# Kernel optimization log

Measured on AMD Instinct MI355X. Metric: run time of the kernel, lower is better.

## Reference

```python
import jax, jax.numpy as jnp
import numpy as np

DIM = 4096
N_HEADS = 32
N_KV_HEADS = 8
HEAD_DIM = DIM // N_HEADS  # 128
B, S = 2, 2048
LN_EPS = 1e-5


def _precompute_freqs_cis(seqlen, head_dim, theta=10000.0):
    inv = 1.0 / (theta ** (np.arange(0, head_dim, 2, dtype=np.float32) / head_dim))  # [HD/2]
    ang = np.outer(np.arange(seqlen, dtype=np.float32), inv)  # [S, HD/2]
    return jnp.asarray(np.stack([np.cos(ang), np.sin(ang)], axis=-1))  # [S, HD/2, 2]


def setup_inputs() -> dict:
    key = jax.random.key(0)
    ks = jax.random.split(key, 9)
    std = 0.02
    return {
        "x": jax.random.normal(ks[0], (B, S, DIM), dtype=jnp.float32),
        "freqs_cis": _precompute_freqs_cis(S, HEAD_DIM),
        "wq": jax.random.normal(ks[1], (N_HEADS * HEAD_DIM, DIM), dtype=jnp.float32) * std,
        "wk": jax.random.normal(ks[2], (N_KV_HEADS * HEAD_DIM, DIM), dtype=jnp.float32) * std,
        "wv": jax.random.normal(ks[3], (N_KV_HEADS * HEAD_DIM, DIM), dtype=jnp.float32) * std,
        "wo": jax.random.normal(ks[4], (DIM, N_HEADS * HEAD_DIM), dtype=jnp.float32) * std,
        "q_norm_w": jnp.ones((N_HEADS * HEAD_DIM,), dtype=jnp.float32),
        "q_norm_b": jnp.zeros((N_HEADS * HEAD_DIM,), dtype=jnp.float32),
        "k_norm_w": jnp.ones((N_KV_HEADS * HEAD_DIM,), dtype=jnp.float32),
        "k_norm_b": jnp.zeros((N_KV_HEADS * HEAD_DIM,), dtype=jnp.float32),
    }


def _layernorm(v, w, b):
    mu = jnp.mean(v, axis=-1, keepdims=True)
    var = jnp.var(v, axis=-1, keepdims=True)
    return (v - mu) * jax.lax.rsqrt(var + LN_EPS) * w + b


def _rope(t, fc):
    # t: [B, S, nh, HD]; fc: [S, HD/2, 2] = (cos, sin)
    b_, s_, nh, hd = t.shape
    tr = t.reshape(b_, s_, nh, hd // 2, 2)
    a, bb = tr[..., 0], tr[..., 1]
    cos = fc[None, :, None, :, 0]
    sin = fc[None, :, None, :, 1]
    out = jnp.stack([a * cos - bb * sin, a * sin + bb * cos], axis=-1)
    return out.reshape(t.shape)


def reference(x, freqs_cis, wq, wk, wv, wo, q_norm_w, q_norm_b, k_norm_w, k_norm_b):
    bsz, seqlen, _ = x.shape
    H, KV, HD = N_HEADS, N_KV_HEADS, HEAD_DIM
    R = H // KV  # GQA repeat factor

    xq = jnp.einsum('bsd,ed->bse', x, wq)
    xk = jnp.einsum('bsd,ed->bse', x, wk)
    xv = jnp.einsum('bsd,ed->bse', x, wv)

    xq = _layernorm(xq, q_norm_w, q_norm_b)
    xk = _layernorm(xk, k_norm_w, k_norm_b)

    xq = xq.reshape(bsz, seqlen, H, HD)
    xk = xk.reshape(bsz, seqlen, KV, HD)
    xv = xv.reshape(bsz, seqlen, KV, HD)

    xq = _rope(xq, freqs_cis)
    xk = _rope(xk, freqs_cis)

    # GQA: group q heads as (kv, rep) and broadcast k/v instead of materializing repeats
    xqg = xq.reshape(bsz, seqlen, KV, R, HD)
    scale = 1.0 / jnp.sqrt(jnp.float32(HD))
    scores = jnp.einsum('bqkrh,bskh->bkrqs', xqg, xk) * scale  # [B,KV,R,S,S]
    attn = jax.nn.softmax(scores, axis=-1)
    out = jnp.einsum('bkrqs,bskh->bqkrh', attn, xv).reshape(bsz, seqlen, H * HD)
    return jnp.einsum('bse,de->bsd', out, wo)
```

## Files before the change

kernel.cpp:

```cpp
#include <hip/hip_runtime.h>
#include <cstdint>

typedef _Float16 half4v __attribute__((ext_vector_type(4)));
typedef _Float16 half8v __attribute__((ext_vector_type(8)));
typedef __fp16   fp16x2 __attribute__((ext_vector_type(2)));
typedef float    f32x4v __attribute__((ext_vector_type(4)));

#define DIM    4096
#define SEQ    2048
#define NBATCH 2
#define NHEAD  32
#define NKVH   8
#define HDIM   128
#define MROWS  (NBATCH*SEQ)
#define QKV_N  6144
#define KOFF   4096
#define VOFF   5120

__device__ __forceinline__ void gl_lds16(const void* g, void* l) {
  __builtin_amdgcn_global_load_lds(
      (const __attribute__((address_space(1))) void*)g,
      (__attribute__((address_space(3))) void*)l, 16, 0, 0);
}

__global__ __launch_bounds__(256) void cvt_kernel(const float* __restrict__ in,
                                                  _Float16* __restrict__ out, int n8) {
  int stride = gridDim.x * blockDim.x;
  for (int i = blockIdx.x * blockDim.x + threadIdx.x; i < n8; i += stride) {
    const float4* p = (const float4*)(in + (size_t)i * 8);
    float4 a = p[0], b = p[1];
    half8v h;
    h[0] = (_Float16)a.x; h[1] = (_Float16)a.y; h[2] = (_Float16)a.z; h[3] = (_Float16)a.w;
    h[4] = (_Float16)b.x; h[5] = (_Float16)b.y; h[6] = (_Float16)b.z; h[7] = (_Float16)b.w;
    *(half8v*)(out + (size_t)i * 8) = h;
  }
}


#define SBAR() do { asm volatile("" ::: "memory"); \
                    __builtin_amdgcn_s_barrier();  \
                    asm volatile("" ::: "memory"); } while (0)
#define LGK0() asm volatile("s_waitcnt lgkmcnt(0)" ::: "memory")
#define VM6()  asm volatile("s_waitcnt vmcnt(6)" ::: "memory")
#define VM2()  asm volatile("s_waitcnt vmcnt(2)" ::: "memory")
#define VM0()  asm volatile("s_waitcnt vmcnt(0)" ::: "memory")

#define STAGE_HALF(Gm, rowbase, kidx, h, buf) do {                                   \
    gl_lds16((Gm) + (size_t)((rowbase) + (h)*128 + srow) * K + (kidx)*64 + sslot8,   \
             (buf) + (h)*8192 + w*512);                                              \
    gl_lds16((Gm) + (size_t)((rowbase) + (h)*128 + 64 + srow) * K + (kidx)*64 + sslot8, \
             (buf) + (h)*8192 + 4096 + w*512);                                       \
  } while (0)

#define MFMA_Q(hm, hn, bf)                                                   \
    _Pragma("unroll") for (int kk = 0; kk < 2; ++kk)                         \
      _Pragma("unroll") for (int mi = 0; mi < 4; ++mi)                       \
        _Pragma("unroll") for (int ni = 0; ni < 2; ++ni)                     \
          acc[(hm) * 4 + mi][(hn) * 2 + ni] =                                \
              __builtin_amdgcn_mfma_f32_16x16x32_f16(                        \
                  a[mi][kk], bf[ni][kk], acc[(hm) * 4 + mi][(hn) * 2 + ni], 0, 0, 0)

#define KSTEP(kcur, AC, BC, AN)                                              \
  do {                                                                       \
    const int k_ = (kcur);                                                   \
    half8v a[4][2], b0[2][2], b1[2][2];                                      \
                                         \
    _Pragma("unroll") for (int mi = 0; mi < 4; ++mi)                         \
      _Pragma("unroll") for (int kk = 0; kk < 2; ++kk)                       \
        a[mi][kk] = *(const half8v*)((AC) + (wm * 128 + mi * 16 + li) * 64 + \
                                     (((kk * 4 + g) ^ li7) * 8));            \
    _Pragma("unroll") for (int ni = 0; ni < 2; ++ni)                         \
      _Pragma("unroll") for (int kk = 0; kk < 2; ++kk)                       \
        b0[ni][kk] = *(const half8v*)((BC) + (wn * 64 + ni * 16 + li) * 64 + \
                                      (((kk * 4 + g) ^ li7) * 8));           \
    if (k_ + 1 < nkt) STAGE_HALF(A, bm, k_ + 1, 1, (AN));                    \
    SBAR(); LGK0();                                                          \
    __builtin_amdgcn_s_setprio(1);                                           \
    MFMA_Q(0, 0, b0);                                                        \
    __builtin_amdgcn_s_setprio(0);                                           \
    SBAR();                                                                  \
                                         \
    _Pragma("unroll") for (int ni = 0; ni < 2; ++ni)                         \
      _Pragma("unroll") for (int kk = 0; kk < 2; ++kk)                       \
        b1[ni][kk] = *(const half8v*)((BC) + (wn * 64 + 32 + ni * 16 + li) * 64 + \
                                      (((kk * 4 + g) ^ li7) * 8));           \
    SBAR(); LGK0();                                                          \
    __builtin_amdgcn_s_setprio(1);                                           \
    MFMA_Q(0, 1, b1);                                                        \
    __builtin_amdgcn_s_setprio(0);                                           \
    SBAR();                                                                  \
          \
    _Pragma("unroll") for (int mi = 0; mi < 4; ++mi)                         \
      _Pragma("unroll") for (int kk = 0; kk < 2; ++kk)                       \
        a[mi][kk] = *(const half8v*)((AC) + (wm * 128 + 64 + mi * 16 + li) * 64 + \
                                     (((kk * 4 + g) ^ li7) * 8));            \
    if (k_ + 2 < nkt) {                                                      \
      STAGE_HALF(B, bn, k_ + 2, 0, (BC));                                    \
      STAGE_HALF(B, bn, k_ + 2, 1, (BC));                                    \
    }                                                                        \
    SBAR(); LGK0();                                                          \
    __builtin_amdgcn_s_setprio(1);                                           \
    MFMA_Q(1, 1, b1);                                                        \
    __builtin_amdgcn_s_setprio(0);                                           \
    SBAR();                                                                  \
          \
    if (k_ + 2 < nkt) STAGE_HALF(A, bm, k_ + 2, 0, (AC));                    \
    SBAR();                                                                  \
    __builtin_amdgcn_s_setprio(1);                                           \
    MFMA_Q(1, 0, b0);                                                        \
    __builtin_amdgcn_s_setprio(0);                                           \
    if (k_ + 2 < nkt) { VM6(); } else if (k_ + 1 < nkt) { VM0(); }           \
    SBAR();                                                                  \
  } while (0)

template<int OUTF16>
__global__ __launch_bounds__(512, 2) void gemm256(const _Float16* __restrict__ A,
                                                  const _Float16* __restrict__ B,
                                                  void* __restrict__ Cp,
                                                  int N, int K, int nbx) {
  __shared__ __align__(16) _Float16 As[2][256 * 64];
  __shared__ __align__(16) _Float16 Bs[2][256 * 64];
  const int tid = threadIdx.x, lane = tid & 63, w = tid >> 6;
  const int g = lane >> 4, li = lane & 15, li7 = lane & 7;
  const int wm = w >> 2, wn = w & 3;
  const int nwg = gridDim.x, orig = blockIdx.x;
  const int wgid = (nwg & 7) ? orig : ((orig & 7) * (nwg >> 3) + (orig >> 3));
  const int bm = (wgid / nbx) * 256, bn = (wgid % nbx) * 256;
  const int srow = tid >> 3;
  const int sslot8 = ((lane & 7) ^ ((lane >> 3) & 7)) * 8;
  const int nkt = K >> 6;
  _Float16* As0 = &As[0][0]; _Float16* As1 = &As[1][0];
  _Float16* Bs0 = &Bs[0][0]; _Float16* Bs1 = &Bs[1][0];

  f32x4v acc[8][4] = {};

  STAGE_HALF(A, bm, 0, 0, As0);
  STAGE_HALF(A, bm, 0, 1, As0);
  STAGE_HALF(B, bn, 0, 0, Bs0);
  STAGE_HALF(B, bn, 0, 1, Bs0);
  if (nkt > 1) {
    STAGE_HALF(B, bn, 1, 0, Bs1);
    STAGE_HALF(B, bn, 1, 1, Bs1);
    STAGE_HALF(A, bm, 1, 0, As1);
    VM6();
  } else {
    VM0();
  }
  SBAR();

  for (int k = 0; k < nkt; k += 2) {
    KSTEP(k,     As0, Bs0, As1);
    KSTEP(k + 1, As1, Bs1, As0);
  }

  const int r0 = bm + wm * 128 + g * 4;
  const int c0 = bn + wn * 64 + li;
#pragma unroll
  for (int mi = 0; mi < 8; ++mi)
#pragma unroll
    for (int ni = 0; ni < 4; ++ni)
#pragma unroll
      for (int j = 0; j < 4; ++j) {
        size_t idx = (size_t)(r0 + mi * 16 + j) * N + (c0 + ni * 16);
        if (OUTF16) ((_Float16*)Cp)[idx] = (_Float16)acc[mi][ni][j];
        else        ((float*)Cp)[idx]    = acc[mi][ni][j];
      }
}

template<int E>
__global__ __launch_bounds__(256) void ln_rope(_Float16* __restrict__ t, int ldt,
                                               const float* __restrict__ gw,
                                               const float* __restrict__ gb,
                                               const float* __restrict__ fc) {
  constexpr int EPT = E / 256;
  const int row = blockIdx.x;
  const int s = row & (SEQ - 1);
  const int tid = threadIdx.x, lane = tid & 63, w = tid >> 6;
  _Float16* rp = t + (size_t)row * ldt + tid * EPT;
  float v[EPT];
#pragma unroll
  for (int i = 0; i < EPT; i += 4) {
    half4v hv = *(const half4v*)(rp + i);
    v[i] = (float)hv[0]; v[i+1] = (float)hv[1]; v[i+2] = (float)hv[2]; v[i+3] = (float)hv[3];
  }
  float sum = 0.f, ssq = 0.f;
#pragma unroll
  for (int i = 0; i < EPT; ++i) { sum += v[i]; ssq += v[i] * v[i]; }
#pragma unroll
  for (int off = 1; off < 64; off <<= 1) { sum += __shfl_xor(sum, off); ssq += __shfl_xor(ssq, off); }
  __shared__ float red[8];
  if (lane == 0) { red[w] = sum; red[4 + w] = ssq; }
  __syncthreads();
  sum = red[0] + red[1] + red[2] + red[3];
  ssq = red[4] + red[5] + red[6] + red[7];
  const float mu = sum * (1.0f / E);
  const float rstd = rsqrtf(ssq * (1.0f / E) - mu * mu + 1e-5f);
  float ov[EPT];
#pragma unroll
  for (int i = 0; i < EPT; i += 2) {
    int e = tid * EPT + i;
    int hd = e & (HDIM - 1);
    float2 cs = *(const float2*)(fc + (size_t)s * HDIM + (hd >> 1) * 2);
    float a = (v[i]   - mu) * rstd * gw[e]   + gb[e];
    float b = (v[i+1] - mu) * rstd * gw[e+1] + gb[e+1];
    ov[i]   = a * cs.x - b * cs.y;
    ov[i+1] = a * cs.y + b * cs.x;
  }
#pragma unroll
  for (int i = 0; i < EPT; i += 4) {
    half4v hv;
    hv[0] = (_Float16)ov[i];   hv[1] = (_Float16)ov[i+1];
    hv[2] = (_Float16)ov[i+2]; hv[3] = (_Float16)ov[i+3];
    *(half4v*)(rp + i) = hv;
  }
}

__global__ __launch_bounds__(256) void vtrans(const _Float16* __restrict__ qkv,
                                              _Float16* __restrict__ vt) {
  __shared__ _Float16 tile[64][136];
  const int blk = blockIdx.x;
  const int st = blk & 31, kvh = (blk >> 5) & 7, b = blk >> 8;
  const int t = threadIdx.x;
  const _Float16* src = qkv + (size_t)(b * SEQ + st * 64) * QKV_N + VOFF + kvh * 128;
#pragma unroll
  for (int i = 0; i < 4; ++i) {
    int sl = (t >> 4) + i * 16;
    int h0 = (t & 15) * 8;
    *(half8v*)&tile[sl][h0] = *(const half8v*)(src + (size_t)sl * QKV_N + h0);
  }
  __syncthreads();
  const int hd = t & 127, half = t >> 7;
  _Float16* dst = vt + ((size_t)((b * NKVH + kvh) * 128 + hd)) * SEQ + st * 64 + half * 32;
#pragma unroll
  for (int j = 0; j < 32; j += 8) {
    half8v v;
#pragma unroll
    for (int e = 0; e < 8; ++e) v[e] = tile[half * 32 + j + e][hd];
    *(half8v*)(dst + j) = v;
  }
}

__global__ __launch_bounds__(512, 4) void attn_kernel(const _Float16* __restrict__ QKV,
                                                      const _Float16* __restrict__ VT,
                                                      _Float16* __restrict__ Oa) {
  __shared__ __align__(16) _Float16 Ksh[2][64 * 128];
  __shared__ __align__(16) char Vsh[128 * 128];
  const int tid = threadIdx.x, lane = tid & 63, w = tid >> 6;
  const int g = lane >> 4, li = lane & 15;
  const int blk = blockIdx.x;
  const int qt = blk & 15, h = (blk >> 4) & 31, b = blk >> 9;
  const int kvh = h >> 2;
  const size_t LD = QKV_N;
  const _Float16* Qb = QKV + (size_t)(b * SEQ) * LD + h * HDIM;
  const _Float16* Kb = QKV + (size_t)(b * SEQ) * LD + KOFF + kvh * HDIM;
  const _Float16* VTb = VT + (size_t)((b * NKVH + kvh) * 128) * SEQ;
  const int lg = lane >> 4;
  const int gbit = (lane >> 5) & 1;

  const int qrow = qt * 128 + w * 16 + li;
  half8v qf[4];
#pragma unroll
  for (int kk = 0; kk < 4; ++kk) {
    half8v q0 = *(const half8v*)(Qb + (size_t)qrow * LD + kk * 32 + g * 8);
#pragma unroll
    for (int e = 0; e < 8; ++e) q0[e] = q0[e] * (_Float16)0.08838834764831845f;
    qf[kk] = q0;
  }
  float mrow = -1e30f, lrow = 0.f;
  f32x4v oacc[8] = {};

#define ASTAGE_K(kt_, buf_) do {                                              \
    _Pragma("unroll") for (int i_ = 0; i_ < 2; ++i_) {                        \
      int chunk = i_ * 8 + w;                                                 \
      int r = chunk * 4 + lg;                                                 \
      int sc8 = ((lane & 15) ^ (r & 7)) * 8;                                  \
      gl_lds16(Kb + (size_t)((kt_) * 64 + r) * LD + sc8, (buf_) + chunk * 512); \
    } } while (0)

#define ASTAGE_V(kt_, buf_) do {                                              \
    _Pragma("unroll") for (int i_ = 0; i_ < 2; ++i_) {                        \
      int chunk = i_ * 8 + w;                                                 \
      int hd_ = chunk * 8 + (lane >> 3);                                      \
      int keyh = (chunk ^ (lane >> 3)) & 7;                                   \
      int p_ = lane & 7;                                                      \
      gl_lds16(VTb + (size_t)hd_ * SEQ + (kt_) * 64 + ((p_ ^ keyh) * 8),      \
               (buf_) + chunk * 1024);                                        \
    } } while (0)

  ASTAGE_K(0, Ksh[0]);
  ASTAGE_V(0, Vsh);
  VM0();
  SBAR();

  const int NT = SEQ / 64;
  for (int kt = 0; kt < NT; ++kt) {
    const int cur = kt & 1;
    const _Float16* Kcur = Ksh[cur];
    f32x4v sc[4] = {};
    __builtin_amdgcn_s_setprio(1);
#pragma unroll
    for (int kk = 0; kk < 4; ++kk) {
#pragma unroll
      for (int ni = 0; ni < 4; ++ni) {
        half8v kf = *(const half8v*)(Kcur + (16 * ni + li) * 128 + ((4 * kk + g) ^ (li & 7)) * 8);
        sc[ni] = __builtin_amdgcn_mfma_f32_16x16x32_f16(kf, qf[kk], sc[ni], 0, 0, 0);
      }
    }
    __builtin_amdgcn_s_setprio(0);
    if (kt + 1 < NT) ASTAGE_K(kt + 1, Ksh[cur ^ 1]);
    float m16 = sc[0][0];
#pragma unroll
    for (int ni = 0; ni < 4; ++ni) {
      m16 = fmaxf(m16, fmaxf(fmaxf(sc[ni][0], sc[ni][1]), fmaxf(sc[ni][2], sc[ni][3])));
    }
    m16 = fmaxf(m16, __shfl_xor(m16, 16));
    m16 = fmaxf(m16, __shfl_xor(m16, 32));
    if (!__all(m16 - mrow <= 8.0f)) {
      const float mn = fmaxf(mrow, m16);
      const float sfo = __expf(mrow - mn);
      mrow = mn;
      lrow *= sfo;
      float sfj[4];
#pragma unroll
      for (int j = 0; j < 4; ++j) sfj[j] = __shfl(sfo, (lane & 48) | (4 * g + j));
#pragma unroll
      for (int nio = 0; nio < 8; ++nio) {
        oacc[nio][0] *= sfj[0]; oacc[nio][1] *= sfj[1];
        oacc[nio][2] *= sfj[2]; oacc[nio][3] *= sfj[3];
      }
    }
    float rs = 0.f;
#pragma unroll
    for (int ni = 0; ni < 4; ++ni)
#pragma unroll
      for (int j = 0; j < 4; ++j) { float pv = __expf(sc[ni][j] - mrow); sc[ni][j] = pv; rs += pv; }
    rs += __shfl_xor(rs, 16); rs += __shfl_xor(rs, 32);
    lrow += rs;
    uint32_t u[4][2];
#pragma unroll
    for (int ni = 0; ni < 4; ++ni) {
      fp16x2 p0 = __builtin_amdgcn_cvt_pkrtz(sc[ni][0], sc[ni][1]);
      fp16x2 p1 = __builtin_amdgcn_cvt_pkrtz(sc[ni][2], sc[ni][3]);
      u[ni][0] = *(uint32_t*)&p0;
      u[ni][1] = *(uint32_t*)&p1;
    }
    if (kt + 1 < NT) { VM2(); } else { VM0(); }
    SBAR();
#pragma unroll
    for (int kk = 0; kk < 2; ++kk) {
      uint32_t own0 = gbit ? u[2*kk+1][0] : u[2*kk][0];
      uint32_t own1 = gbit ? u[2*kk+1][1] : u[2*kk][1];
      uint32_t oth0 = gbit ? u[2*kk][0]   : u[2*kk+1][0];
      uint32_t oth1 = gbit ? u[2*kk][1]   : u[2*kk+1][1];
      uint32_t r16_0 = (uint32_t)__shfl_xor((int)own0, 16);
      uint32_t r16_1 = (uint32_t)__shfl_xor((int)own1, 16);
      uint32_t r32_0 = (uint32_t)__shfl_xor((int)oth0, 32);
      uint32_t r32_1 = (uint32_t)__shfl_xor((int)oth1, 32);
      uint32_t r48_0 = (uint32_t)__shfl_xor((int)oth0, 48);
      uint32_t r48_1 = (uint32_t)__shfl_xor((int)oth1, 48);
      uint32_t d0 = (g == 0) ? own0 : (g == 1) ? r48_0 : (g == 2) ? r32_0 : r16_0;
      uint32_t d1 = (g == 0) ? own1 : (g == 1) ? r48_1 : (g == 2) ? r32_1 : r16_1;
      uint32_t d2 = (g == 0) ? r16_0 : (g == 1) ? r32_0 : (g == 2) ? r48_0 : own0;
      uint32_t d3 = (g == 0) ? r16_1 : (g == 1) ? r32_1 : (g == 2) ? r48_1 : own1;
      union { uint32_t u4[4]; half8v hh; } pa;
      pa.u4[0] = d0; pa.u4[1] = d1; pa.u4[2] = d2; pa.u4[3] = d3;
      __builtin_amdgcn_s_setprio(1);
#pragma unroll
      for (int nio = 0; nio < 8; ++nio) {
        int r = nio * 16 + li;
        int key = ((r >> 3) ^ r) & 7;
        half8v bv = *(const half8v*)(Vsh + r * 128 + (((kk * 4 + g) ^ key) << 4));
        oacc[nio] = __builtin_amdgcn_mfma_f32_16x16x32_f16(pa.hh, bv, oacc[nio], 0, 0, 0);
      }
      __builtin_amdgcn_s_setprio(0);
    }
    VM0();
    SBAR();
    if (kt + 1 < NT) ASTAGE_V(kt + 1, Vsh);
  }
#undef ASTAGE_K
#undef ASTAGE_V
  float rinv[4];
#pragma unroll
  for (int j = 0; j < 4; ++j)
    rinv[j] = 1.0f / __shfl(lrow, (lane & 48) | (4 * g + j));
  _Float16* Ob = Oa + (size_t)(b * SEQ + qt * 128 + w * 16) * DIM + h * HDIM;
#pragma unroll
  for (int j = 0; j < 4; ++j)
#pragma unroll
    for (int nio = 0; nio < 8; ++nio)
      Ob[(size_t)(4 * g + j) * DIM + nio * 16 + li] = (_Float16)(oacc[nio][j] * rinv[j]);
}

extern "C" void kernel_launch(void* const* d_in, const int* in_sizes, int n_in,
                              void* d_out, int out_size, void* d_ws, size_t ws_size,
                              hipStream_t stream) {
  const float* x   = (const float*)d_in[0];
  const float* fc  = (const float*)d_in[1];
  const float* wq  = (const float*)d_in[2];
  const float* wk  = (const float*)d_in[3];
  const float* wv  = (const float*)d_in[4];
  const float* wo  = (const float*)d_in[5];
  const float* qnw = (const float*)d_in[6];
  const float* qnb = (const float*)d_in[7];
  const float* knw = (const float*)d_in[8];
  const float* knb = (const float*)d_in[9];
  float* out = (float*)d_out;
  (void)in_sizes; (void)n_in; (void)out_size;

  const size_t MB = 1024 * 1024;
  if (ws_size < 128 * MB) return;
  char* ws = (char*)d_ws;
  _Float16* x_h    = (_Float16*)(ws + 0);
  _Float16* wqkv_h = (_Float16*)(ws + 32 * MB);
  _Float16* wk_h   = (_Float16*)(ws + 64 * MB);
  _Float16* wv_h   = (_Float16*)(ws + 72 * MB);
  _Float16* qkv_h  = (_Float16*)(ws + 80 * MB);
  _Float16* wo_h   = wqkv_h;
  _Float16* vt_h   = wk_h;
  _Float16* ao_h   = x_h;

  cvt_kernel<<<2048, 256, 0, stream>>>(x,  x_h,    (MROWS * DIM) / 8);
  cvt_kernel<<<2048, 256, 0, stream>>>(wq, wqkv_h, (DIM * DIM) / 8);
  cvt_kernel<<<1024, 256, 0, stream>>>(wk, wk_h,   (1024 * DIM) / 8);
  cvt_kernel<<<1024, 256, 0, stream>>>(wv, wv_h,   (1024 * DIM) / 8);

  gemm256<1><<<(MROWS / 256) * (QKV_N / 256), 512, 0, stream>>>(x_h, wqkv_h, qkv_h,
                                                                QKV_N, DIM, QKV_N / 256);

  cvt_kernel<<<2048, 256, 0, stream>>>(wo, wo_h, (DIM * DIM) / 8);

  vtrans<<<NBATCH * NKVH * (SEQ / 64), 256, 0, stream>>>(qkv_h, vt_h);

  ln_rope<4096><<<MROWS, 256, 0, stream>>>(qkv_h,        QKV_N, qnw, qnb, fc);
  ln_rope<1024><<<MROWS, 256, 0, stream>>>(qkv_h + KOFF, QKV_N, knw, knb, fc);

  attn_kernel<<<NBATCH * NHEAD * (SEQ / 128), 512, 0, stream>>>(qkv_h, vt_h, ao_h);

  gemm256<0><<<(MROWS / 256) * (DIM / 256), 512, 0, stream>>>(ao_h, wo_h, out,
                                                              DIM, DIM, DIM / 256);
}
```

Before: 655.0 us.

## Use 128x256 tiled GEMM with two blocks per CU for QKV projection

Adds a gemm128 kernel that uses 128-row M tiles instead of 256, with a reworked staged-load and MFMA interleaving schedule and launch bounds targeting two workgroups per CU. The QKV projection now launches twice as many workgroups (768 instead of 384), aiming for better CU fill across the 256 CUs and less tail imbalance. In exchange, each B tile is reused across fewer rows, which raises global and LDS traffic per FLOP. The output projection still uses the original gemm256.

```diff
diff --git a/kernel.cpp b/kernel.cpp
--- a/kernel.cpp
+++ b/kernel.cpp
@@ -36,12 +36,12 @@
   }
 }
 
-
 #define SBAR() do { asm volatile("" ::: "memory"); \
                     __builtin_amdgcn_s_barrier();  \
                     asm volatile("" ::: "memory"); } while (0)
 #define LGK0() asm volatile("s_waitcnt lgkmcnt(0)" ::: "memory")
 #define VM6()  asm volatile("s_waitcnt vmcnt(6)" ::: "memory")
+#define VM5()  asm volatile("s_waitcnt vmcnt(5)" ::: "memory")
 #define VM2()  asm volatile("s_waitcnt vmcnt(2)" ::: "memory")
 #define VM0()  asm volatile("s_waitcnt vmcnt(0)" ::: "memory")
 
@@ -167,6 +167,131 @@
       }
 }
 
+#define STAGE_U(Gm, rowbase, kidx, h, buf)                                      \
+    gl_lds16((Gm) + (size_t)((rowbase) + (h)*64 + srow) * K + (kidx)*64 + sslot8, \
+             (buf) + (h)*4096 + w*512)
+
+#define MFMA_Q2(mb, nb, af, bf)                                              \
+    _Pragma("unroll") for (int kk = 0; kk < 2; ++kk)                         \
+      _Pragma("unroll") for (int mi = 0; mi < 2; ++mi)                       \
+        _Pragma("unroll") for (int ni = 0; ni < 2; ++ni)                     \
+          acc[(mb) + mi][(nb) + ni] =                                        \
+              __builtin_amdgcn_mfma_f32_16x16x32_f16(                        \
+                  af[mi][kk], bf[ni][kk], acc[(mb) + mi][(nb) + ni], 0, 0, 0)
+
+#define KSTEP2(kcur, AC, BC, AN)                                             \
+  do {                                                                       \
+    const int k_ = (kcur);                                                   \
+    half8v al[2][2], ah[2][2], b0[2][2], b1[2][2];                           \
+                                             \
+    _Pragma("unroll") for (int mi = 0; mi < 2; ++mi)                         \
+      _Pragma("unroll") for (int kk = 0; kk < 2; ++kk)                       \
+        al[mi][kk] = *(const half8v*)((AC) + (wm * 64 + mi * 16 + li) * 64 + \
+                                      (((kk * 4 + g) ^ li7) * 8));           \
+    _Pragma("unroll") for (int ni = 0; ni < 2; ++ni)                         \
+      _Pragma("unroll") for (int kk = 0; kk < 2; ++kk)                       \
+        b0[ni][kk] = *(const half8v*)((BC) + (wn * 64 + ni * 16 + li) * 64 + \
+                                      (((kk * 4 + g) ^ li7) * 8));           \
+    if (k_ + 1 < nkt) STAGE_U(A, bm, k_ + 1, 1, (AN));                       \
+    SBAR(); LGK0();                                                          \
+    __builtin_amdgcn_s_setprio(1);                                           \
+    MFMA_Q2(0, 0, al, b0);                                                   \
+    __builtin_amdgcn_s_setprio(0);                                           \
+    SBAR();                                                                  \
+                                             \
+    _Pragma("unroll") for (int ni = 0; ni < 2; ++ni)                         \
+      _Pragma("unroll") for (int kk = 0; kk < 2; ++kk)                       \
+        b1[ni][kk] = *(const half8v*)((BC) + (wn * 64 + 32 + ni * 16 + li) * 64 + \
+                                      (((kk * 4 + g) ^ li7) * 8));           \
+    SBAR(); LGK0();                                                          \
+    __builtin_amdgcn_s_setprio(1);                                           \
+    MFMA_Q2(0, 2, al, b1);                                                   \
+    __builtin_amdgcn_s_setprio(0);                                           \
+    SBAR();                                                                  \
+              \
+    _Pragma("unroll") for (int mi = 0; mi < 2; ++mi)                         \
+      _Pragma("unroll") for (int kk = 0; kk < 2; ++kk)                       \
+        ah[mi][kk] = *(const half8v*)((AC) + (wm * 64 + 32 + mi * 16 + li) * 64 + \
+                                      (((kk * 4 + g) ^ li7) * 8));           \
+    if (k_ + 2 < nkt) {                                                      \
+      STAGE_U(B, bn, k_ + 2, 0, (BC));                                       \
+      STAGE_U(B, bn, k_ + 2, 1, (BC));                                       \
+      STAGE_U(B, bn, k_ + 2, 2, (BC));                                       \
+      STAGE_U(B, bn, k_ + 2, 3, (BC));                                       \
+    }                                                                        \
+    SBAR(); LGK0();                                                          \
+    __builtin_amdgcn_s_setprio(1);                                           \
+    MFMA_Q2(2, 2, ah, b1);                                                   \
+    __builtin_amdgcn_s_setprio(0);                                           \
+    SBAR();                                                                  \
+              \
+    if (k_ + 2 < nkt) STAGE_U(A, bm, k_ + 2, 0, (AC));                       \
+    SBAR();                                                                  \
+    __builtin_amdgcn_s_setprio(1);                                           \
+    MFMA_Q2(2, 0, ah, b0);                                                   \
+    __builtin_amdgcn_s_setprio(0);                                           \
+    if (k_ + 2 < nkt) { VM5(); } else if (k_ + 1 < nkt) { VM0(); }           \
+    SBAR();                                                                  \
+  } while (0)
+
+template<int OUTF16>
+__global__ __launch_bounds__(512, 2) void gemm128(const _Float16* __restrict__ A,
+                                                  const _Float16* __restrict__ B,
+                                                  void* __restrict__ Cp,
+                                                  int N, int K, int nbx) {
+  __shared__ __align__(16) _Float16 As[2][128 * 64];
+  __shared__ __align__(16) _Float16 Bs[2][256 * 64];
+  const int tid = threadIdx.x, lane = tid & 63, w = tid >> 6;
+  const int g = lane >> 4, li = lane & 15, li7 = lane & 7;
+  const int wm = w >> 2, wn = w & 3;
+  const int nwg = gridDim.x, orig = blockIdx.x;
+  const int wgid = (nwg & 7) ? orig : ((orig & 7) * (nwg >> 3) + (orig >> 3));
+  const int bm = (wgid / nbx) * 128, bn = (wgid % nbx) * 256;
+  const int srow = tid >> 3;
+  const int sslot8 = ((lane & 7) ^ ((lane >> 3) & 7)) * 8;
+  const int nkt = K >> 6;
+  _Float16* As0 = &As[0][0]; _Float16* As1 = &As[1][0];
+  _Float16* Bs0 = &Bs[0][0]; _Float16* Bs1 = &Bs[1][0];
+
+  f32x4v acc[4][4] = {};
+
+  STAGE_U(A, bm, 0, 0, As0);
+  STAGE_U(A, bm, 0, 1, As0);
+  STAGE_U(B, bn, 0, 0, Bs0);
+  STAGE_U(B, bn, 0, 1, Bs0);
+  STAGE_U(B, bn, 0, 2, Bs0);
+  STAGE_U(B, bn, 0, 3, Bs0);
+  if (nkt > 1) {
+    STAGE_U(B, bn, 1, 0, Bs1);
+    STAGE_U(B, bn, 1, 1, Bs1);
+    STAGE_U(B, bn, 1, 2, Bs1);
+    STAGE_U(B, bn, 1, 3, Bs1);
+    STAGE_U(A, bm, 1, 0, As1);
+    VM5();
+  } else {
+    VM0();
+  }
+  SBAR();
+
+  for (int k = 0; k < nkt; k += 2) {
+    KSTEP2(k,     As0, Bs0, As1);
+    KSTEP2(k + 1, As1, Bs1, As0);
+  }
+
+  const int r0 = bm + wm * 64 + g * 4;
+  const int c0 = bn + wn * 64 + li;
+#pragma unroll
+  for (int mi = 0; mi < 4; ++mi)
+#pragma unroll
+    for (int ni = 0; ni < 4; ++ni)
+#pragma unroll
+      for (int j = 0; j < 4; ++j) {
+        size_t idx = (size_t)(r0 + mi * 16 + j) * N + (c0 + ni * 16);
+        if (OUTF16) ((_Float16*)Cp)[idx] = (_Float16)acc[mi][ni][j];
+        else        ((float*)Cp)[idx]    = acc[mi][ni][j];
+      }
+}
+
 template<int E>
 __global__ __launch_bounds__(256) void ln_rope(_Float16* __restrict__ t, int ldt,
                                                const float* __restrict__ gw,
@@ -425,7 +550,7 @@
   cvt_kernel<<<1024, 256, 0, stream>>>(wk, wk_h,   (1024 * DIM) / 8);
   cvt_kernel<<<1024, 256, 0, stream>>>(wv, wv_h,   (1024 * DIM) / 8);
 
-  gemm256<1><<<(MROWS / 256) * (QKV_N / 256), 512, 0, stream>>>(x_h, wqkv_h, qkv_h,
+  gemm128<1><<<(MROWS / 128) * (QKV_N / 256), 512, 0, stream>>>(x_h, wqkv_h, qkv_h,
                                                                 QKV_N, DIM, QKV_N / 256);
 
   cvt_kernel<<<2048, 256, 0, stream>>>(wo, wo_h, (DIM * DIM) / 8);
```

After: 668.6 us. 2.1% more time.
